# Performance work log

Measured on AMD Instinct MI355X. Metric: run time of the kernel, lower is better.

Reference implementation:

```python
import jax, jax.numpy as jnp
import numpy as np

HIDDEN = 2048
N_HEADS = 16
N_KV_HEADS = 8
HEAD_DIM = 128
ROTARY_DIM = 32  # int(128 * 0.25), already even
ROPE_THETA = 10000000.0
EPS = 1e-6
BATCH, SEQ = 2, 2048


def _rmsnorm(x, w, eps=EPS):
    # per-head RMSNorm over last dim; weight is zero-init, scale = 1 + w
    r = jax.lax.rsqrt(jnp.mean(x * x, axis=-1, keepdims=True) + eps)
    return x * r * (1.0 + w)


def _rope(x, positions, rotary_dim, theta):
    # x: [b, s, h, rotary_dim]; rotate-halves RoPE
    half = rotary_dim // 2
    inv_freq = 1.0 / (theta ** (jnp.arange(half, dtype=jnp.float32) / half))
    ang = positions.astype(jnp.float32)[:, :, None] * inv_freq  # [b, s, half]
    cos = jnp.cos(ang)[:, :, None, :]
    sin = jnp.sin(ang)[:, :, None, :]
    x1, x2 = x[..., :half], x[..., half:]
    return jnp.concatenate([x1 * cos - x2 * sin, x1 * sin + x2 * cos], axis=-1)


def setup_inputs() -> dict:
    key = jax.random.key(0)
    ks = jax.random.split(key, 8)
    scale = lambda fan_in: 1.0 / np.sqrt(fan_in)
    x = jax.random.normal(ks[0], (BATCH, SEQ, HIDDEN), dtype=jnp.float32)
    Wq = jax.random.normal(ks[1], (HIDDEN, N_HEADS * HEAD_DIM * 2), jnp.float32) * scale(HIDDEN)
    Wk = jax.random.normal(ks[2], (HIDDEN, N_KV_HEADS * HEAD_DIM), jnp.float32) * scale(HIDDEN)
    Wv = jax.random.normal(ks[3], (HIDDEN, N_KV_HEADS * HEAD_DIM), jnp.float32) * scale(HIDDEN)
    Wo = jax.random.normal(ks[4], (N_HEADS * HEAD_DIM, HIDDEN), jnp.float32) * scale(N_HEADS * HEAD_DIM)
    q_norm_w = jax.random.normal(ks[5], (HEAD_DIM,), jnp.float32) * 0.02
    k_norm_w = jax.random.normal(ks[6], (HEAD_DIM,), jnp.float32) * 0.02
    attention_mask = jnp.ones((BATCH, SEQ), dtype=jnp.int32)
    positions = jnp.broadcast_to(jnp.arange(SEQ, dtype=jnp.int32), (BATCH, SEQ))
    return {"x": x, "attention_mask": attention_mask, "positions": positions,
            "Wq": Wq, "Wk": Wk, "Wv": Wv, "Wo": Wo,
            "q_norm_w": q_norm_w, "k_norm_w": k_norm_w}


def reference(x, attention_mask, positions, Wq, Wk, Wv, Wo, q_norm_w, k_norm_w):
    b, s, _ = x.shape
    g = N_HEADS // N_KV_HEADS  # GQA group size

    q_all = jnp.einsum('bsh,ho->bso', x, Wq).reshape(b, s, N_HEADS, HEAD_DIM * 2)
    q, gate = jnp.split(q_all, 2, axis=-1)          # each [b,s,H,D]
    gate = gate.reshape(b, s, N_HEADS * HEAD_DIM)
    q = _rmsnorm(q, q_norm_w)
    k = _rmsnorm(jnp.einsum('bsh,ho->bso', x, Wk).reshape(b, s, N_KV_HEADS, HEAD_DIM), k_norm_w)
    v = jnp.einsum('bsh,ho->bso', x, Wv).reshape(b, s, N_KV_HEADS, HEAD_DIM)

    # partial RoPE on first ROTARY_DIM dims
    q = jnp.concatenate([_rope(q[..., :ROTARY_DIM], positions, ROTARY_DIM, ROPE_THETA), q[..., ROTARY_DIM:]], axis=-1)
    k = jnp.concatenate([_rope(k[..., :ROTARY_DIM], positions, ROTARY_DIM, ROPE_THETA), k[..., ROTARY_DIM:]], axis=-1)

    # grouped-query causal attention
    qg = q.reshape(b, s, N_KV_HEADS, g, HEAD_DIM)
    scores = jnp.einsum('bqhgd,bkhd->bhgqk', qg, k) / jnp.sqrt(jnp.float32(HEAD_DIM))
    causal = jnp.tril(jnp.ones((s, s), dtype=bool))
    key_valid = attention_mask.astype(bool)[:, None, None, None, :]  # [b,1,1,1,k]
    mask = causal[None, None, None, :, :] & key_valid
    scores = jnp.where(mask, scores, jnp.finfo(scores.dtype).min)
    probs = jax.nn.softmax(scores, axis=-1)
    attn = jnp.einsum('bhgqk,bkhd->bqhgd', probs, v).reshape(b, s, N_HEADS * HEAD_DIM)

    attn = attn * jax.nn.sigmoid(gate)
    return jnp.einsum('bso,oh->bsh', attn, Wo)
```

## Files before the change

kernel.cpp:

```cpp
#include <hip/hip_runtime.h>
#include <cstdint>

typedef __bf16  bf16;
typedef __bf16  bf16x8 __attribute__((ext_vector_type(8)));
typedef __bf16  bf16x4 __attribute__((ext_vector_type(4)));
typedef __bf16  bf16x2 __attribute__((ext_vector_type(2)));
typedef float   f32x4  __attribute__((ext_vector_type(4)));
typedef float   f32x16 __attribute__((ext_vector_type(16)));

#define GLOAD_LDS16(g, l) __builtin_amdgcn_global_load_lds( \
    (const __attribute__((address_space(1))) void*)(g),     \
    (__attribute__((address_space(3))) void*)(l), 16, 0, 0)

#define SEQ   2048
#define HID   2048
#define NH    16
#define NKV   8
#define HD    128
#define NQKV  6144
#define MTOT  4096

__device__ __forceinline__ void transw_body(const float* __restrict__ W, bf16* __restrict__ WT,
                                            int N, int n0, int k0, int t) {
    __shared__ float tile[64][65];
    int tn = t & 63, t4 = t >> 6;
    #pragma unroll
    for (int i = 0; i < 16; ++i) {
        int kk = i * 4 + t4;
        tile[kk][tn] = W[(size_t)(k0 + kk) * N + n0 + tn];
    }
    __syncthreads();
    #pragma unroll
    for (int i = 0; i < 16; ++i) {
        int nn = i * 4 + t4;
        WT[(size_t)(n0 + nn) * HID + k0 + tn] = (bf16)tile[tn][nn];
    }
}

__global__ __launch_bounds__(256) void prep_kernel(const float* __restrict__ x, bf16* __restrict__ xb,
                                                   const float* __restrict__ Wq, const float* __restrict__ Wk,
                                                   const float* __restrict__ Wv, const float* __restrict__ Wo,
                                                   bf16* __restrict__ wqkvT, bf16* __restrict__ woT) {
    int bx = blockIdx.x, t = threadIdx.x;
    if (bx < 8192) {
        int i = bx * 256 + t;
        f32x4 v = ((const f32x4*)x)[i];
        bf16x4 o;
        o[0] = (bf16)v[0]; o[1] = (bf16)v[1]; o[2] = (bf16)v[2]; o[3] = (bf16)v[3];
        ((bf16x4*)xb)[i] = o;
    } else if (bx < 8192 + 2048) {
        int idx = bx - 8192;
        transw_body(Wq, wqkvT, 4096, (idx & 63) * 64, (idx >> 6) * 64, t);
    } else if (bx < 8192 + 2048 + 512) {
        int idx = bx - (8192 + 2048);
        transw_body(Wk, wqkvT + (size_t)4096 * HID, 1024, (idx & 15) * 64, (idx >> 4) * 64, t);
    } else if (bx < 8192 + 2048 + 1024) {
        int idx = bx - (8192 + 2048 + 512);
        transw_body(Wv, wqkvT + (size_t)5120 * HID, 1024, (idx & 15) * 64, (idx >> 4) * 64, t);
    } else {
        int idx = bx - (8192 + 2048 + 1024);
        transw_body(Wo, woT, 2048, (idx & 31) * 64, (idx >> 5) * 64, t);
    }
}

template<bool OUT_BF16>
__global__ __launch_bounds__(256) void gemm_bt(const bf16* __restrict__ A, const bf16* __restrict__ Bt,
                                               void* __restrict__ C, int M, int N, int K) {
    __shared__ __align__(16) bf16 As[128 * 64];
    __shared__ __align__(16) bf16 Bs[128 * 64];
    const int tid = threadIdx.x;
    const int wave = tid >> 6, lane = tid & 63;
    const int l31 = lane & 31, half = lane >> 5;
    const int tile_n = blockIdx.x * 128, tile_m = blockIdx.y * 128;
    const int wm = (wave & 1) * 64, wn = (wave >> 1) * 64;
    const int sw = l31 & 7;
    f32x16 acc[2][2] = {};

    for (int k0 = 0; k0 < K; k0 += 64) {
        __syncthreads();
        #pragma unroll
        for (int j = 0; j < 4; ++j) {
            int s = j * 256 + tid;
            int row = s >> 3, c = s & 7;
            int cs = c ^ (row & 7);
            GLOAD_LDS16(A  + (size_t)(tile_m + row) * K + k0 + (cs << 3), As + (size_t)s * 8);
            GLOAD_LDS16(Bt + (size_t)(tile_n + row) * K + k0 + (cs << 3), Bs + (size_t)s * 8);
        }
        __syncthreads();
        #pragma unroll
        for (int ks = 0; ks < 4; ++ks) {
            int ch = ((ks * 2 + half) ^ sw) << 3;
            bf16x8 a0 = *(const bf16x8*)(As + (size_t)(wm + l31) * 64 + ch);
            bf16x8 a1 = *(const bf16x8*)(As + (size_t)(wm + 32 + l31) * 64 + ch);
            bf16x8 b0 = *(const bf16x8*)(Bs + (size_t)(wn + l31) * 64 + ch);
            bf16x8 b1 = *(const bf16x8*)(Bs + (size_t)(wn + 32 + l31) * 64 + ch);
            acc[0][0] = __builtin_amdgcn_mfma_f32_32x32x16_bf16(a0, b0, acc[0][0], 0, 0, 0);
            acc[0][1] = __builtin_amdgcn_mfma_f32_32x32x16_bf16(a0, b1, acc[0][1], 0, 0, 0);
            acc[1][0] = __builtin_amdgcn_mfma_f32_32x32x16_bf16(a1, b0, acc[1][0], 0, 0, 0);
            acc[1][1] = __builtin_amdgcn_mfma_f32_32x32x16_bf16(a1, b1, acc[1][1], 0, 0, 0);
        }
    }
    #pragma unroll
    for (int mt = 0; mt < 2; ++mt)
        #pragma unroll
        for (int nt = 0; nt < 2; ++nt)
            #pragma unroll
            for (int reg = 0; reg < 16; ++reg) {
                int row = tile_m + wm + mt * 32 + (reg & 3) + ((reg >> 2) * 8) + half * 4;
                int col = tile_n + wn + nt * 32 + l31;
                float v = acc[mt][nt][reg];
                if (OUT_BF16) ((bf16*)C)[(size_t)row * N + col] = (bf16)v;
                else          ((float*)C)[(size_t)row * N + col] = v;
            }
}

__global__ __launch_bounds__(256) void post_kernel(const bf16* __restrict__ qkv,
                                                   const float* __restrict__ qnw, const float* __restrict__ knw,
                                                   const int* __restrict__ positions,
                                                   bf16* __restrict__ Qh, bf16* __restrict__ Kh,
                                                   bf16* __restrict__ VT) {
    int bx = blockIdx.x;
    if (bx < 4096) {
        int tk = bx;
        int b = tk >> 11, s = tk & 2047;
        int wave = threadIdx.x >> 6, lane = threadIdx.x & 63;
        int e0 = lane * 2, e1 = e0 + 1;
        float pos = (float)positions[tk];
        const float L = 1.4533435415278355f;
        float a0 = pos * exp2f(-(float)(e0 & 15) * L);
        float a1 = pos * exp2f(-(float)(e1 & 15) * L);
        float cv0 = cosf(a0), sv0 = sinf(a0);
        float cv1 = cosf(a1), sv1 = sinf(a1);
        float qw0 = 1.0f + qnw[e0], qw1 = 1.0f + qnw[e1];
        float kw0 = 1.0f + knw[e0], kw1 = 1.0f + knw[e1];

        #pragma unroll
        for (int i = 0; i < 6; ++i) {
            bool isq = (i < 4);
            int h = wave + (isq ? i : (i - 4)) * 4;
            const bf16* base = qkv + (size_t)tk * NQKV + (isq ? h * 256 : 4096 + h * HD);
            bf16x2 v = *(const bf16x2*)(base + e0);
            float f0 = (float)v[0], f1 = (float)v[1];
            float ssq = f0 * f0 + f1 * f1;
            #pragma unroll
            for (int off = 32; off; off >>= 1) ssq += __shfl_xor(ssq, off);
            float rn = rsqrtf(ssq * (1.0f / 128.0f) + 1e-6f);
            float w0 = isq ? qw0 : kw0, w1 = isq ? qw1 : kw1;
            float x0 = f0 * rn * w0, x1 = f1 * rn * w1;
            float p0 = __shfl_xor(x0, 8), p1 = __shfl_xor(x1, 8);
            float r0 = x0, r1 = x1;
            if (lane < 8)       { r0 = x0 * cv0 - p0 * sv0; r1 = x1 * cv1 - p1 * sv1; }
            else if (lane < 16) { r0 = p0 * sv0 + x0 * cv0; r1 = p1 * sv1 + x1 * cv1; }
            bf16x2 o; o[0] = (bf16)r0; o[1] = (bf16)r1;
            bf16* dst = isq ? (Qh + ((size_t)(b * NH + h) * SEQ + s) * HD)
                            : (Kh + ((size_t)(b * NKV + h) * SEQ + s) * HD);
            *(bf16x2*)(dst + e0) = o;
        }
    } else {
        int idx = bx - 4096;
        int bh = idx >> 5, st = idx & 31;
        int b = bh >> 3, h = bh & 7;
        __shared__ float tile[64][129];
        int t = threadIdx.x;
        const bf16* src = qkv + ((size_t)(b * SEQ) + st * 64) * NQKV + 5120 + h * HD;
        #pragma unroll
        for (int i = 0; i < 32; ++i) {
            int ii = i * 256 + t;
            int tok = ii >> 7, d = ii & 127;
            tile[tok][d] = (float)src[(size_t)tok * NQKV + d];
        }
        __syncthreads();
        bf16* dst = VT + (size_t)(b * NKV + h) * HD * SEQ + st * 64;
        #pragma unroll
        for (int i = 0; i < 32; ++i) {
            int ii = i * 256 + t;
            int d = ii >> 6, sx = ii & 63;
            dst[(size_t)d * SEQ + sx] = (bf16)tile[sx][d];
        }
    }
}

__global__ __launch_bounds__(512, 4) void attn_kernel(const bf16* __restrict__ Qh, const bf16* __restrict__ Kh,
                                                      const bf16* __restrict__ VT, const bf16* __restrict__ qkv,
                                                      const int* __restrict__ amask, bf16* __restrict__ attnb) {
    const int bx = blockIdx.x;
    const int hb = (bx >> 4) & 31;
    const int head = hb & 15, b = hb >> 4;
    int q0 = ((bx & 15) + hb) & 15;
    const int qt = (bx & 256) ? (15 - q0) : q0;
    const int kvh = head >> 1;
    __shared__ __align__(16) bf16 Ks[64 * 128];
    __shared__ __align__(16) bf16 Vs[128 * 64];
    __shared__ __align__(16) bf16 Ps[8 * 16 * 64];
    const int tid = threadIdx.x, wave = tid >> 6, lane = tid & 63;
    const int quad = lane >> 4, cl = lane & 15;

    const bf16* qsrc = Qh + ((size_t)(b * NH + head) * SEQ + qt * 128) * HD;
    bf16x8 aq[4];
    #pragma unroll
    for (int kc = 0; kc < 4; ++kc)
        aq[kc] = *(const bf16x8*)(qsrc + (size_t)(wave * 16 + cl) * HD + kc * 32 + quad * 8);

    float lstate[4] = {0.0f, 0.0f, 0.0f, 0.0f};
    f32x4 oacc[8] = {};
    const int qrow_glob = qt * 128 + wave * 16 + quad * 4;
    const float scale = 0.08838834764831845f * 1.4426950408889634f;
    const float M = 20.0f;
    const int kmax = 2 * qt + 1;

    for (int kt = 0; kt <= kmax; ++kt) {
        __syncthreads();
        const bf16* ksrc = Kh + ((size_t)(b * NKV + kvh) * SEQ + kt * 64) * HD;
        const bf16* vsrc = VT + (size_t)(b * NKV + kvh) * HD * SEQ + kt * 64;
        #pragma unroll
        for (int j = 0; j < 2; ++j) {
            int s = j * 512 + tid;
            int rK = s >> 4, cK = s & 15;
            GLOAD_LDS16(ksrc + (size_t)rK * HD + ((cK ^ (rK & 15)) << 3), Ks + (size_t)s * 8);
            int dV = s >> 3, cV = s & 7;
            GLOAD_LDS16(vsrc + (size_t)dV * SEQ + ((cV ^ (dV & 7)) << 3), Vs + (size_t)s * 8);
        }
        __syncthreads();

        f32x4 sc[4] = {};
        #pragma unroll
        for (int nt = 0; nt < 4; ++nt)
            #pragma unroll
            for (int kc = 0; kc < 4; ++kc) {
                bf16x8 bk = *(const bf16x8*)(Ks + (size_t)(nt * 16 + cl) * 128 + (((kc * 4 + quad) ^ cl) << 3));
                sc[nt] = __builtin_amdgcn_mfma_f32_16x16x32_bf16(aq[kc], bk, sc[nt], 0, 0, 0);
            }

        #pragma unroll
        for (int nt = 0; nt < 4; ++nt) {
            int kcol = kt * 64 + nt * 16 + cl;
            bool cok = (amask[b * SEQ + kcol] != 0);
            #pragma unroll
            for (int r = 0; r < 4; ++r) {
                bool ok = cok && (kcol <= qrow_glob + r);
                float p = ok ? exp2f(sc[nt][r] * scale - M) : 0.0f;
                lstate[r] += p;
                Ps[wave * 1024 + (quad * 4 + r) * 64 + ((nt * 16 + cl) ^ (quad << 4))] = (bf16)p;
            }
        }

        bf16x8 ap[2];
        #pragma unroll
        for (int c = 0; c < 2; ++c)
            ap[c] = *(const bf16x8*)(Ps + wave * 1024 + cl * 64 + ((c * 32 + quad * 8) ^ ((cl >> 2) << 4)));
        #pragma unroll
        for (int n2 = 0; n2 < 8; ++n2)
            #pragma unroll
            for (int c = 0; c < 2; ++c) {
                bf16x8 bv = *(const bf16x8*)(Vs + (size_t)(n2 * 16 + cl) * 64 + (((c * 4 + quad) ^ (cl & 7)) << 3));
                oacc[n2] = __builtin_amdgcn_mfma_f32_16x16x32_bf16(ap[c], bv, oacc[n2], 0, 0, 0);
            }
    }

    #pragma unroll
    for (int r = 0; r < 4; ++r) {
        #pragma unroll
        for (int off = 8; off; off >>= 1) lstate[r] += __shfl_xor(lstate[r], off);
        int srow = qt * 128 + wave * 16 + quad * 4 + r;
        float linv = 1.0f / lstate[r];
        #pragma unroll
        for (int n2 = 0; n2 < 8; ++n2) {
            int d = n2 * 16 + cl;
            float g = (float)qkv[(size_t)(b * SEQ + srow) * NQKV + head * 256 + 128 + d];
            float sig = 1.0f / (1.0f + __expf(-g));
            float v = oacc[n2][r] * linv * sig;
            attnb[(size_t)(b * SEQ + srow) * HID + head * HD + d] = (bf16)v;
        }
    }
}

extern "C" void kernel_launch(void* const* d_in, const int* in_sizes, int n_in,
                              void* d_out, int out_size, void* d_ws, size_t ws_size,
                              hipStream_t stream) {
    const float* x        = (const float*)d_in[0];
    const int*   amask    = (const int*)d_in[1];
    const int*   positions= (const int*)d_in[2];
    const float* Wq       = (const float*)d_in[3];
    const float* Wk       = (const float*)d_in[4];
    const float* Wv       = (const float*)d_in[5];
    const float* Wo       = (const float*)d_in[6];
    const float* qnw      = (const float*)d_in[7];
    const float* knw      = (const float*)d_in[8];
    float* out = (float*)d_out;
    char* ws = (char*)d_ws;

    bf16* xb    = (bf16*)(ws);
    bf16* wqkvT = (bf16*)(ws + 16777216);
    bf16* woT   = (bf16*)(ws + 41943040);
    bf16* qkv   = (bf16*)(ws + 50331648);
    bf16* Qh    = (bf16*)(ws + 100663296);
    bf16* Kh    = (bf16*)(ws + 117440512);
    bf16* VT    = (bf16*)(ws + 125829120);
    bf16* attnb = (bf16*)(ws + 134217728);

    prep_kernel<<<12288, 256, 0, stream>>>(x, xb, Wq, Wk, Wv, Wo, wqkvT, woT);
    gemm_bt<true><<<dim3(48, 32), 256, 0, stream>>>(xb, wqkvT, qkv, MTOT, NQKV, HID);
    post_kernel<<<4608, 256, 0, stream>>>(qkv, qnw, knw, positions, Qh, Kh, VT);
    attn_kernel<<<512, 512, 0, stream>>>(Qh, Kh, VT, qkv, amask, attnb);
    gemm_bt<false><<<dim3(16, 32), 256, 0, stream>>>(attnb, woT, out, MTOT, HID, HID);

    (void)in_sizes; (void)n_in; (void)out_size; (void)ws_size;
}
```

Before: 402.0 us.

## Replace QKV projection GEMM with 256x256 tile, 8-wave pipelined MFMA kernel

Adds a new gemm256 kernel for the QKV projection. It uses 256x256 output tiles, 512 threads and 16x16x32 bf16 MFMAs, and stages A and B quarter-tiles into double-buffered swizzled LDS with direct global-to-LDS loads. The loads are interleaved with MFMA phases under fine-grained barriers, vmcnt waits and setprio. The aim is to raise data reuse per tile and hide global-load latency behind compute. The cost is 128 KB of LDS per block, larger register pressure, and only 24x16=384 blocks to fill the GPU.

```diff
diff --git a/kernel.cpp b/kernel.cpp
--- a/kernel.cpp
+++ b/kernel.cpp
@@ -114,6 +114,146 @@
             }
 }
 
+__device__ __forceinline__ void stageA256(const bf16* __restrict__ A, int tile_m, int K,
+                                          int t, int h, bf16* dst, int tid) {
+    int k0 = t << 6;
+    #pragma unroll
+    for (int j = 0; j < 2; ++j) {
+        int s = j * 512 + tid;
+        int wr = s >> 3, c = s & 7;
+        int cs = c ^ (wr & 7);
+        int gr = ((wr >> 6) << 7) | (h << 6) | (wr & 63);
+        GLOAD_LDS16(A + (size_t)(tile_m + gr) * K + k0 + (cs << 3), dst + (size_t)s * 8);
+    }
+}
+__device__ __forceinline__ void stageB256(const bf16* __restrict__ Bt, int tile_n, int K,
+                                          int t, int h, bf16* dst, int tid) {
+    int k0 = t << 6;
+    #pragma unroll
+    for (int j = 0; j < 2; ++j) {
+        int s = j * 512 + tid;
+        int wr = s >> 3, c = s & 7;
+        int cs = c ^ (wr & 7);
+        int gr = ((wr >> 5) << 6) | (h << 5) | (wr & 31);
+        GLOAD_LDS16(Bt + (size_t)(tile_n + gr) * K + k0 + (cs << 3), dst + (size_t)s * 8);
+    }
+}
+
+__global__ __launch_bounds__(512, 2) void gemm256(const bf16* __restrict__ A, const bf16* __restrict__ Bt,
+                                                  bf16* __restrict__ C, int M, int N, int K) {
+    __shared__ __align__(16) bf16 As[2][2][128 * 64];
+    __shared__ __align__(16) bf16 Bs[2][2][128 * 64];
+    const int tid = threadIdx.x;
+    const int wave = tid >> 6, lane = tid & 63;
+    const int l15 = lane & 15, quad = lane >> 4;
+    const int wrow = wave >> 2, wcol = wave & 3;
+    const int tile_n = blockIdx.x * 256, tile_m = blockIdx.y * 256;
+
+    f32x4 acc[8][4] = {};
+    bf16x8 aF[4][2], bF[2][2];
+
+#define LOAD_AF(sl, mh) { \
+    const bf16* _ba = &As[sl][mh][0]; \
+    _Pragma("unroll") for (int mf2 = 0; mf2 < 4; ++mf2) \
+    _Pragma("unroll") for (int ks = 0; ks < 2; ++ks) { \
+        int wr = wrow * 64 + mf2 * 16 + l15; \
+        int pc = (ks * 4 + quad) ^ (l15 & 7); \
+        aF[mf2][ks] = *(const bf16x8*)(_ba + wr * 64 + pc * 8); \
+    } }
+#define LOAD_BF(sl, nh) { \
+    const bf16* _bb = &Bs[sl][nh][0]; \
+    _Pragma("unroll") for (int nf2 = 0; nf2 < 2; ++nf2) \
+    _Pragma("unroll") for (int ks = 0; ks < 2; ++ks) { \
+        int wr = wcol * 32 + nf2 * 16 + l15; \
+        int pc = (ks * 4 + quad) ^ (l15 & 7); \
+        bF[nf2][ks] = *(const bf16x8*)(_bb + wr * 64 + pc * 8); \
+    } }
+#define MIDBAR() { __builtin_amdgcn_s_barrier(); \
+    asm volatile("s_waitcnt lgkmcnt(0)" ::: "memory"); \
+    __builtin_amdgcn_sched_barrier(0); }
+#define MFMA16(mh, nh) { \
+    __builtin_amdgcn_s_setprio(1); \
+    _Pragma("unroll") for (int mf2 = 0; mf2 < 4; ++mf2) \
+    _Pragma("unroll") for (int nf2 = 0; nf2 < 2; ++nf2) \
+    _Pragma("unroll") for (int ks = 0; ks < 2; ++ks) \
+        acc[(mh)*4+mf2][(nh)*2+nf2] = __builtin_amdgcn_mfma_f32_16x16x32_bf16( \
+            aF[mf2][ks], bF[nf2][ks], acc[(mh)*4+mf2][(nh)*2+nf2], 0, 0, 0); \
+    __builtin_amdgcn_s_setprio(0); }
+#define ENDBAR() __builtin_amdgcn_s_barrier();
+#define VMCNT6() asm volatile("s_waitcnt vmcnt(6)" ::: "memory");
+#define VMCNT0() asm volatile("s_waitcnt vmcnt(0)" ::: "memory");
+
+    const int NITER = K >> 7;
+
+    stageA256(A,  tile_m, K, 0, 0, &As[0][0][0], tid);
+    stageB256(Bt, tile_n, K, 0, 0, &Bs[0][0][0], tid);
+    stageB256(Bt, tile_n, K, 0, 1, &Bs[0][1][0], tid);
+    stageA256(A,  tile_m, K, 0, 1, &As[0][1][0], tid);
+    stageA256(A,  tile_m, K, 1, 0, &As[1][0][0], tid);
+    stageB256(Bt, tile_n, K, 1, 1, &Bs[1][1][0], tid);
+    stageA256(A,  tile_m, K, 1, 1, &As[1][1][0], tid);
+    VMCNT6();
+    __builtin_amdgcn_s_barrier();
+
+    for (int it = 0; it < NITER - 1; ++it) {
+        const int T = 2 * it;
+        LOAD_AF(0, 0); LOAD_BF(0, 0);
+        stageB256(Bt, tile_n, K, T + 1, 0, &Bs[1][0][0], tid);
+        MIDBAR(); MFMA16(0, 0); ENDBAR();
+        LOAD_BF(0, 1);
+        stageA256(A, tile_m, K, T + 2, 0, &As[0][0][0], tid);
+        MIDBAR(); MFMA16(0, 1); ENDBAR();
+        LOAD_AF(0, 1);
+        stageB256(Bt, tile_n, K, T + 2, 1, &Bs[0][1][0], tid);
+        MIDBAR(); MFMA16(1, 1); ENDBAR();
+        LOAD_BF(0, 0);
+        stageA256(A, tile_m, K, T + 2, 1, &As[0][1][0], tid);
+        MIDBAR(); MFMA16(1, 0); VMCNT6(); ENDBAR();
+        LOAD_AF(1, 0); LOAD_BF(1, 0);
+        stageB256(Bt, tile_n, K, T + 2, 0, &Bs[0][0][0], tid);
+        MIDBAR(); MFMA16(0, 0); ENDBAR();
+        LOAD_BF(1, 1);
+        stageA256(A, tile_m, K, T + 3, 0, &As[1][0][0], tid);
+        MIDBAR(); MFMA16(0, 1); ENDBAR();
+        LOAD_AF(1, 1);
+        stageB256(Bt, tile_n, K, T + 3, 1, &Bs[1][1][0], tid);
+        MIDBAR(); MFMA16(1, 1); ENDBAR();
+        LOAD_BF(1, 0);
+        stageA256(A, tile_m, K, T + 3, 1, &As[1][1][0], tid);
+        MIDBAR(); MFMA16(1, 0); VMCNT6(); ENDBAR();
+    }
+    {
+        LOAD_AF(0, 0); LOAD_BF(0, 0);
+        stageB256(Bt, tile_n, K, 2 * NITER - 1, 0, &Bs[1][0][0], tid);
+        MIDBAR(); MFMA16(0, 0); ENDBAR();
+        LOAD_BF(0, 1); MIDBAR(); MFMA16(0, 1); ENDBAR();
+        LOAD_AF(0, 1); MIDBAR(); MFMA16(1, 1); ENDBAR();
+        LOAD_BF(0, 0); MIDBAR(); MFMA16(1, 0); VMCNT0(); ENDBAR();
+        LOAD_AF(1, 0); LOAD_BF(1, 0); MIDBAR(); MFMA16(0, 0); ENDBAR();
+        LOAD_BF(1, 1); MIDBAR(); MFMA16(0, 1); ENDBAR();
+        LOAD_AF(1, 1); MIDBAR(); MFMA16(1, 1); ENDBAR();
+        LOAD_BF(1, 0); MIDBAR(); MFMA16(1, 0); ENDBAR();
+    }
+
+    #pragma unroll
+    for (int mf = 0; mf < 8; ++mf)
+        #pragma unroll
+        for (int nf = 0; nf < 4; ++nf)
+            #pragma unroll
+            for (int r = 0; r < 4; ++r) {
+                int row = tile_m + wrow * 128 + mf * 16 + quad * 4 + r;
+                int col = tile_n + wcol * 64 + nf * 16 + l15;
+                C[(size_t)row * N + col] = (bf16)acc[mf][nf][r];
+            }
+#undef LOAD_AF
+#undef LOAD_BF
+#undef MIDBAR
+#undef MFMA16
+#undef ENDBAR
+#undef VMCNT6
+#undef VMCNT0
+}
+
 __global__ __launch_bounds__(256) void post_kernel(const bf16* __restrict__ qkv,
                                                    const float* __restrict__ qnw, const float* __restrict__ knw,
                                                    const int* __restrict__ positions,
@@ -299,7 +439,7 @@
     bf16* attnb = (bf16*)(ws + 134217728);
 
     prep_kernel<<<12288, 256, 0, stream>>>(x, xb, Wq, Wk, Wv, Wo, wqkvT, woT);
-    gemm_bt<true><<<dim3(48, 32), 256, 0, stream>>>(xb, wqkvT, qkv, MTOT, NQKV, HID);
+    gemm256<<<dim3(NQKV / 256, MTOT / 256), 512, 0, stream>>>(xb, wqkvT, qkv, MTOT, NQKV, HID);
     post_kernel<<<4608, 256, 0, stream>>>(qkv, qnw, knw, positions, Qh, Kh, VT);
     attn_kernel<<<512, 512, 0, stream>>>(Qh, Kh, VT, qkv, amask, attnb);
     gemm_bt<false><<<dim3(16, 32), 256, 0, stream>>>(attnb, woT, out, MTOT, HID, HID);
```

Measured after the change: 413.1 us. 2.8% more time.

## Double-buffer K/V tiles in attention kernel to overlap loads with MFMA

Applied to the files above, without the earlier changes.

The K and V shared-memory tiles become two-deep buffers. The next tile's global-to-LDS async loads are issued right after the per-iteration barrier, so they run while the current tile's QK and PV MFMAs execute, and the second barrier per iteration goes away. This is meant to hide global load latency. The cost is 32KB more LDS per block, which lowers how many blocks fit on each CU.

```diff
diff --git a/kernel.cpp b/kernel.cpp
--- a/kernel.cpp
+++ b/kernel.cpp
@@ -189,8 +189,8 @@
     int q0 = ((bx & 15) + hb) & 15;
     const int qt = (bx & 256) ? (15 - q0) : q0;
     const int kvh = head >> 1;
-    __shared__ __align__(16) bf16 Ks[64 * 128];
-    __shared__ __align__(16) bf16 Vs[128 * 64];
+    __shared__ __align__(16) bf16 Ks[2][64 * 128];
+    __shared__ __align__(16) bf16 Vs[2][128 * 64];
     __shared__ __align__(16) bf16 Ps[8 * 16 * 64];
     const int tid = threadIdx.x, wave = tid >> 6, lane = tid & 63;
     const int quad = lane >> 4, cl = lane & 15;
@@ -208,26 +208,33 @@
     const float M = 20.0f;
     const int kmax = 2 * qt + 1;
 
+    const bf16* kbase = Kh + (size_t)(b * NKV + kvh) * SEQ * HD;
+    const bf16* vbase = VT + (size_t)(b * NKV + kvh) * HD * SEQ;
+
+#define STAGE_KV(kt_, buf_) { \
+    const bf16* ksrc = kbase + (size_t)(kt_) * 64 * HD; \
+    const bf16* vsrc = vbase + (size_t)(kt_) * 64; \
+    _Pragma("unroll") \
+    for (int j = 0; j < 2; ++j) { \
+        int s = j * 512 + tid;                     \
+        int rK = s >> 4, cK = s & 15; \
+        GLOAD_LDS16(ksrc + (size_t)rK * HD + ((cK ^ (rK & 15)) << 3), &Ks[buf_][0] + (size_t)s * 8); \
+        int dV = s >> 3, cV = s & 7; \
+        GLOAD_LDS16(vsrc + (size_t)dV * SEQ + ((cV ^ (dV & 7)) << 3), &Vs[buf_][0] + (size_t)s * 8); \
+    } }
+
+    STAGE_KV(0, 0);
+    int cur = 0;
     for (int kt = 0; kt <= kmax; ++kt) {
         __syncthreads();
-        const bf16* ksrc = Kh + ((size_t)(b * NKV + kvh) * SEQ + kt * 64) * HD;
-        const bf16* vsrc = VT + (size_t)(b * NKV + kvh) * HD * SEQ + kt * 64;
-        #pragma unroll
-        for (int j = 0; j < 2; ++j) {
-            int s = j * 512 + tid;
-            int rK = s >> 4, cK = s & 15;
-            GLOAD_LDS16(ksrc + (size_t)rK * HD + ((cK ^ (rK & 15)) << 3), Ks + (size_t)s * 8);
-            int dV = s >> 3, cV = s & 7;
-            GLOAD_LDS16(vsrc + (size_t)dV * SEQ + ((cV ^ (dV & 7)) << 3), Vs + (size_t)s * 8);
-        }
-        __syncthreads();
+        if (kt < kmax) STAGE_KV(kt + 1, cur ^ 1);
 
         f32x4 sc[4] = {};
         #pragma unroll
         for (int nt = 0; nt < 4; ++nt)
             #pragma unroll
             for (int kc = 0; kc < 4; ++kc) {
-                bf16x8 bk = *(const bf16x8*)(Ks + (size_t)(nt * 16 + cl) * 128 + (((kc * 4 + quad) ^ cl) << 3));
+                bf16x8 bk = *(const bf16x8*)(&Ks[cur][0] + (size_t)(nt * 16 + cl) * 128 + (((kc * 4 + quad) ^ cl) << 3));
                 sc[nt] = __builtin_amdgcn_mfma_f32_16x16x32_bf16(aq[kc], bk, sc[nt], 0, 0, 0);
             }
 
@@ -252,10 +259,12 @@
         for (int n2 = 0; n2 < 8; ++n2)
             #pragma unroll
             for (int c = 0; c < 2; ++c) {
-                bf16x8 bv = *(const bf16x8*)(Vs + (size_t)(n2 * 16 + cl) * 64 + (((c * 4 + quad) ^ (cl & 7)) << 3));
+                bf16x8 bv = *(const bf16x8*)(&Vs[cur][0] + (size_t)(n2 * 16 + cl) * 64 + (((c * 4 + quad) ^ (cl & 7)) << 3));
                 oacc[n2] = __builtin_amdgcn_mfma_f32_16x16x32_bf16(ap[c], bv, oacc[n2], 0, 0, 0);
             }
-    }
+        cur ^= 1;
+    }
+#undef STAGE_KV
 
     #pragma unroll
     for (int r = 0; r < 4; ++r) {
```

Measured after the change: 390.5 us. 2.9% less time.
